# Kernel tuning notes

Measured on AMD Instinct MI355X. Metric: run time of the kernel, lower is better.

The kernel has to match this reference:

```python
import jax, jax.numpy as jnp
import numpy as np
import math

EMBED_DIM = 1024
NUM_HEADS = 16
HEAD_DIM = EMBED_DIM // NUM_HEADS
ROPE_BASE = 10000.0


def setup_inputs() -> dict:
    key = jax.random.key(0)
    ks = jax.random.split(key, 11)
    B, S, E = 2, 2048, EMBED_DIM
    s = 1.0 / math.sqrt(E)
    return {
        "query": jax.random.normal(ks[0], (B, S, E), jnp.float32),
        "key": jax.random.normal(ks[1], (B, S, E), jnp.float32),
        "value": jax.random.normal(ks[2], (B, S, E), jnp.float32),
        "Wq": jax.random.normal(ks[3], (E, E), jnp.float32) * s,
        "bq": jnp.zeros((E,), jnp.float32),
        "Wk": jax.random.normal(ks[4], (E, E), jnp.float32) * s,
        "bk": jnp.zeros((E,), jnp.float32),
        "Wv": jax.random.normal(ks[5], (E, E), jnp.float32) * s,
        "bv": jnp.zeros((E,), jnp.float32),
        "Wo": jax.random.normal(ks[6], (E, E), jnp.float32) * s,
        "bo": jnp.zeros((E,), jnp.float32),
    }


def _rope_cache(S, D, dtype):
    inv_freq = 1.0 / (ROPE_BASE ** (jnp.arange(0, D, 2, dtype=jnp.float32) / D))
    t = jnp.arange(S, dtype=jnp.float32)
    freqs = t[:, None] * inv_freq[None, :]  # [S, D/2]
    return jnp.cos(freqs).astype(dtype), jnp.sin(freqs).astype(dtype)


def _apply_rope(x, cos, sin):
    # x: [B, H, S, D]; cos/sin: [S, D/2]
    x_even = x[..., 0::2]
    x_odd = x[..., 1::2]
    rot_even = x_even * cos - x_odd * sin
    rot_odd = x_odd * cos + x_even * sin
    # interleave back: [..., D/2, 2] -> [..., D]
    return jnp.stack([rot_even, rot_odd], axis=-1).reshape(x.shape)


def reference(query, key, value, Wq, bq, Wk, bk, Wv, bv, Wo, bo):
    B, S, E = query.shape
    H, D = NUM_HEADS, HEAD_DIM
    q = (query @ Wq.T + bq).reshape(B, S, H, D).transpose(0, 2, 1, 3)
    k = (key @ Wk.T + bk).reshape(B, S, H, D).transpose(0, 2, 1, 3)
    v = (value @ Wv.T + bv).reshape(B, S, H, D).transpose(0, 2, 1, 3)
    cos, sin = _rope_cache(S, D, q.dtype)
    q = _apply_rope(q, cos, sin)
    k = _apply_rope(k, cos, sin)
    scores = jnp.einsum('bhsd,bhtd->bhst', q, k) / math.sqrt(D)
    attn = jax.nn.softmax(scores, axis=-1)
    out = jnp.einsum('bhst,bhtd->bhsd', attn, v)
    out = out.transpose(0, 2, 1, 3).reshape(B, S, E)
    return out @ Wo.T + bo
```

## Files before the change

### kernel.cpp

```cpp
#include <hip/hip_runtime.h>
#include <math.h>

typedef unsigned short u16;
typedef __bf16 bf16x8 __attribute__((ext_vector_type(8)));
typedef float floatx4 __attribute__((ext_vector_type(4)));
typedef float floatx16 __attribute__((ext_vector_type(16)));

#define MFMA16(a, b, c) __builtin_amdgcn_mfma_f32_16x16x32_bf16((a), (b), (c), 0, 0, 0)
#define MFMA32(a, b, c) __builtin_amdgcn_mfma_f32_32x32x16_bf16((a), (b), (c), 0, 0, 0)

__device__ __forceinline__ float bf2f(u16 u) {
  union { float f; unsigned int i; } v; v.i = ((unsigned int)u) << 16; return v.f;
}
__device__ __forceinline__ u16 f2bf(float f) {
  __bf16 h = (__bf16)f;
  union { __bf16 h; u16 u; } v; v.h = h; return v.u;
}
__device__ __forceinline__ bf16x8 cvt8(float4 a, float4 b) {
  bf16x8 r;
  r[0] = (__bf16)a.x; r[1] = (__bf16)a.y; r[2] = (__bf16)a.z; r[3] = (__bf16)a.w;
  r[4] = (__bf16)b.x; r[5] = (__bf16)b.y; r[6] = (__bf16)b.z; r[7] = (__bf16)b.w;
  return r;
}
__device__ __forceinline__ void gl2lds16(const void* g, void* l) {
  __builtin_amdgcn_global_load_lds(
      (const __attribute__((address_space(1))) unsigned int*)g,
      (__attribute__((address_space(3))) unsigned int*)l, 16, 0, 0);
}

struct CvtArgs { const float* src[3]; u16* dst[3]; };
__global__ __launch_bounds__(256) void cvt_kernel(CvtArgs a) {
  const float* s = a.src[blockIdx.z];
  u16* d = a.dst[blockIdx.z];
  const int i = (blockIdx.x * 256 + threadIdx.x) * 8;
  const float4 x = *reinterpret_cast<const float4*>(s + i);
  const float4 y = *reinterpret_cast<const float4*>(s + i + 4);
  *reinterpret_cast<bf16x8*>(&d[i]) = cvt8(x, y);
}

struct GemmArgs {
  const void* A[3];
  const void* W[3];
  const float* bias[3];
  void* C[3];
  int out_mode[3];
};

template <int BM, int ABF16, int WBF16>
__global__ __launch_bounds__(256) void gemm_nt(GemmArgs args) {
  const int N = 1024, K = 1024;

  const int NY = gridDim.y;
  const int lin = blockIdx.x + (blockIdx.y << 3) + blockIdx.z * (NY << 3);
  const int chunk = NY * gridDim.z;
  const int nid = (lin & 7) * chunk + (lin >> 3);
  const int z = nid / (NY << 3);
  const int rem = nid - z * (NY << 3);
  const int m0 = (rem >> 3) * BM, n0 = (rem & 7) * 128;

  const float* bias = args.bias[z];
  const int out_mode = args.out_mode[z];
  constexpr int MI = BM / 32;

  __shared__ __align__(16) char AsB[ABF16 ? BM * 64 : BM * 128];
  __shared__ __align__(16) char BsB[WBF16 ? 128 * 64 : 128 * 128];

  const int t = threadIdx.x;
  const int wave = t >> 6, lane = t & 63;
  const int lr = lane & 15, quad = lane >> 4;
  const int wm = (wave >> 1) * (BM / 2), wn = (wave & 1) * 64;

  auto stage = [&](int kt) {
    if constexpr (ABF16) {
      const u16* Ab = (const u16*)args.A[z];
      constexpr int NI = BM / 16;
#pragma unroll
      for (int j = 0; j < (NI + 3) / 4; j++) {
        const int ii = wave + j * 4;
        if (NI >= 4 || ii < NI) {
          const int r0 = ii * 16;
          const int row = r0 + (lane >> 2);
          const int cg = (lane & 3) ^ ((lane >> 2) & 3);
          gl2lds16(Ab + (size_t)(m0 + row) * K + kt + cg * 8, AsB + r0 * 64 + lane * 16);
        }
      }
    } else {
      const float* Af = (const float*)args.A[z];
#pragma unroll
      for (int j = 0; j < BM / 32; j++) {
        const int r0 = wave * (BM / 4) + j * 8;
        const int row = r0 + (lane >> 3);
        const int cg = (lane & 7) ^ ((lane >> 3) & 7);
        gl2lds16(Af + (size_t)(m0 + row) * K + kt + cg * 4, AsB + r0 * 128 + lane * 16);
      }
    }
    if constexpr (WBF16) {
      const u16* Wb = (const u16*)args.W[z];
#pragma unroll
      for (int j = 0; j < 2; j++) {
        const int r0 = (wave + j * 4) * 16;
        const int row = r0 + (lane >> 2);
        const int cg = (lane & 3) ^ ((lane >> 2) & 3);
        gl2lds16(Wb + (size_t)(n0 + row) * K + kt + cg * 8, BsB + r0 * 64 + lane * 16);
      }
    } else {
      const float* Wf = (const float*)args.W[z];
#pragma unroll
      for (int j = 0; j < 4; j++) {
        const int r0 = wave * 32 + j * 8;
        const int row = r0 + (lane >> 3);
        const int cg = (lane & 7) ^ ((lane >> 3) & 7);
        gl2lds16(Wf + (size_t)(n0 + row) * K + kt + cg * 4, BsB + r0 * 128 + lane * 16);
      }
    }
  };

  floatx4 acc[MI][4] = {};

  for (int kt = 0; kt < K; kt += 32) {
    __syncthreads();
    stage(kt);
    __syncthreads();

    bf16x8 af[MI], bf[4];
#pragma unroll
    for (int i = 0; i < MI; i++) {
      const int row = wm + i * 16 + lr;
      if constexpr (ABF16) {
        const int cp = quad ^ (row & 3);
        af[i] = *reinterpret_cast<const bf16x8*>(AsB + row * 64 + cp * 16);
      } else {
        const int e = row & 7;
        const float4 c0 = *reinterpret_cast<const float4*>(AsB + row * 128 + ((2 * quad) ^ e) * 16);
        const float4 c1 = *reinterpret_cast<const float4*>(AsB + row * 128 + ((2 * quad + 1) ^ e) * 16);
        af[i] = cvt8(c0, c1);
      }
    }
#pragma unroll
    for (int i = 0; i < 4; i++) {
      const int row = wn + i * 16 + lr;
      if constexpr (WBF16) {
        const int cp = quad ^ (row & 3);
        bf[i] = *reinterpret_cast<const bf16x8*>(BsB + row * 64 + cp * 16);
      } else {
        const int e = row & 7;
        const float4 c0 = *reinterpret_cast<const float4*>(BsB + row * 128 + ((2 * quad) ^ e) * 16);
        const float4 c1 = *reinterpret_cast<const float4*>(BsB + row * 128 + ((2 * quad + 1) ^ e) * 16);
        bf[i] = cvt8(c0, c1);
      }
    }
#pragma unroll
    for (int mi = 0; mi < MI; mi++)
#pragma unroll
      for (int nf = 0; nf < 4; nf++)
        acc[mi][nf] = MFMA16(af[mi], bf[nf], acc[mi][nf]);
  }

#pragma unroll
  for (int nf = 0; nf < 4; nf++) {
    const int col = n0 + wn + nf * 16 + lr;
    const float bv = bias[col];
#pragma unroll
    for (int mi = 0; mi < MI; mi++) {
      const int row0 = m0 + wm + mi * 16 + quad * 4;
      if (out_mode == 0) {
        u16* C = (u16*)args.C[z];
#pragma unroll
        for (int r = 0; r < 4; r++)
          C[(row0 + r) * N + col] = f2bf(acc[mi][nf][r] + bv);
      } else if (out_mode == 1) {
        u16* C = (u16*)args.C[z];
        const int h = col >> 6, d = col & 63;
        const int b = row0 >> 11, s = row0 & 2047;
        ushort4 pk;
        pk.x = f2bf(acc[mi][nf][0] + bv);
        pk.y = f2bf(acc[mi][nf][1] + bv);
        pk.z = f2bf(acc[mi][nf][2] + bv);
        pk.w = f2bf(acc[mi][nf][3] + bv);
        *reinterpret_cast<ushort4*>(&C[((b * 16 + h) * 64 + d) * 2048 + s]) = pk;
      } else {
        float* C = (float*)args.C[z];
#pragma unroll
        for (int r = 0; r < 4; r++)
          C[(row0 + r) * N + col] = acc[mi][nf][r] + bv;
      }
    }
  }
}

__global__ __launch_bounds__(256) void rope_kernel(u16* Q, u16* Kb) {
  const int idx = blockIdx.x * 256 + threadIdx.x;
  const int tensor = idx >> 19;
  const int i = idx & 524287;
  u16* P = tensor ? Kb : Q;
  const int row = i >> 7;
  const int cg = i & 127;
  const int s = row & 2047;
  const int col0 = cg * 8;
  const float scale = tensor ? 1.0f : 0.18033688011112042f;
  union { uint4 u; u16 h[8]; } v;
  v.u = *reinterpret_cast<const uint4*>(&P[row * 1024 + col0]);
  const int j0 = (col0 & 63) >> 1;
#pragma unroll
  for (int p = 0; p < 4; p++) {
    const int j = j0 + p;
    const float inv = exp2f(-(float)j * (13.287712379549449f / 32.0f));
    const float f = (float)s * inv;
    float sn, cs;
    sincosf(f, &sn, &cs);
    const float e = bf2f(v.h[2 * p]), o = bf2f(v.h[2 * p + 1]);
    v.h[2 * p]     = f2bf((e * cs - o * sn) * scale);
    v.h[2 * p + 1] = f2bf((o * cs + e * sn) * scale);
  }
  *reinterpret_cast<uint4*>(&P[row * 1024 + col0]) = v.u;
}

#define MAKE_PB(pp, g, out) do {                                              \
    unsigned int wA, wB, wC, wD;                                              \
    asm("v_cvt_pk_bf16_f32 %0, %1, %2" : "=v"(wA) : "v"((pp)[(g)+0]), "v"((pp)[(g)+1])); \
    asm("v_cvt_pk_bf16_f32 %0, %1, %2" : "=v"(wB) : "v"((pp)[(g)+4]), "v"((pp)[(g)+5])); \
    asm("v_cvt_pk_bf16_f32 %0, %1, %2" : "=v"(wC) : "v"((pp)[(g)+2]), "v"((pp)[(g)+3])); \
    asm("v_cvt_pk_bf16_f32 %0, %1, %2" : "=v"(wD) : "v"((pp)[(g)+6]), "v"((pp)[(g)+7])); \
    asm("v_permlane32_swap_b32 %0, %1" : "+v"(wA), "+v"(wB));                 \
    asm("v_permlane32_swap_b32 %0, %1" : "+v"(wC), "+v"(wD));                 \
    union { unsigned int w[4]; bf16x8 v; } u_;                                \
    u_.w[0] = wA; u_.w[1] = wC; u_.w[2] = wB; u_.w[3] = wD;                   \
    (out) = u_.v;                                                             \
  } while (0)

__global__ __launch_bounds__(256, 2) void attn_kernel(const u16* Q, const u16* K,
                                                      const u16* Vt, u16* O) {
  const int lin = blockIdx.x + (blockIdx.y << 4);
  const int nid = (lin & 7) * 64 + (lin >> 3);
  const int bx = nid & 15, bh = nid >> 4;

  const int b = bh >> 4, h = bh & 15;
  const int t = threadIdx.x;
  const int warp = t >> 6, lane = t & 63;
  const int lq = lane & 31, hi = lane >> 5;

  __shared__ __align__(16) u16 Ks[2][64][64];
  __shared__ __align__(16) u16 Vs[2][64][64];

  const int q0 = bx * 128 + warp * 32;

  const u16* qp = &Q[(size_t)(b * 2048 + q0 + lq) * 1024 + h * 64 + hi * 8];
  bf16x8 qf[4];
#pragma unroll
  for (int s = 0; s < 4; s++) qf[s] = *reinterpret_cast<const bf16x8*>(&qp[s * 16]);

  const u16* kbase = &K[(size_t)b * 2048 * 1024 + h * 64];
  const u16* vbase = &Vt[(size_t)bh * 131072];

  const int srr = lane >> 3;
  const int scg = (lane & 7) ^ srr;

  auto stage = [&](int kt2, int bufi) {
#pragma unroll
    for (int j = 0; j < 2; j++) {
      const int r0 = warp * 16 + j * 8;
      const int row = r0 + srr;
      gl2lds16(kbase + (size_t)(kt2 + row) * 1024 + scg * 8, &Ks[bufi][r0][0]);
      gl2lds16(vbase + (size_t)row * 2048 + kt2 + scg * 8, &Vs[bufi][r0][0]);
    }
  };

  floatx16 o0 = {}, o1 = {};
  float m = -1.0e30f, l = 0.0f;

  stage(0, 0);
  int buf = 0;
  for (int kt = 0; kt < 2048; kt += 64) {
    __syncthreads();
    if (kt + 64 < 2048) stage(kt + 64, buf ^ 1);

    bf16x8 kf[2][4], vf[4][2];
#pragma unroll
    for (int kb = 0; kb < 2; kb++) {
      const int r = kb * 32 + lq;
#pragma unroll
      for (int s = 0; s < 4; s++)
        kf[kb][s] = *reinterpret_cast<const bf16x8*>(&Ks[buf][r][((s * 2 + hi) ^ (r & 7)) * 8]);
    }
#pragma unroll
    for (int d = 0; d < 2; d++) {
      const int r = d * 32 + lq;
#pragma unroll
      for (int ks = 0; ks < 4; ks++)
        vf[ks][d] = *reinterpret_cast<const bf16x8*>(&Vs[buf][r][((ks * 2 + hi) ^ (r & 7)) * 8]);
    }

    floatx16 p0 = {}, p1 = {};
#pragma unroll
    for (int s = 0; s < 4; s++) {
      p0 = MFMA32(kf[0][s], qf[s], p0);
      p1 = MFMA32(kf[1][s], qf[s], p1);
    }

    float mx = p0[0];
#pragma unroll
    for (int r = 1; r < 16; r++) mx = fmaxf(mx, p0[r]);
#pragma unroll
    for (int r = 0; r < 16; r++) mx = fmaxf(mx, p1[r]);
    mx = fmaxf(mx, __shfl_xor(mx, 32, 64));
    if (!__all(mx <= m + 10.0f)) {
      const float mn = fmaxf(m, mx);
      const float al = __builtin_amdgcn_exp2f(m - mn);
      m = mn;
      l *= al;
#pragma unroll
      for (int r = 0; r < 16; r++) { o0[r] *= al; o1[r] *= al; }
    }
    float sum = 0.0f;
#pragma unroll
    for (int r = 0; r < 16; r++) { p0[r] = __builtin_amdgcn_exp2f(p0[r] - m); sum += p0[r]; }
#pragma unroll
    for (int r = 0; r < 16; r++) { p1[r] = __builtin_amdgcn_exp2f(p1[r] - m); sum += p1[r]; }
    l += sum + __shfl_xor(sum, 32, 64);

    bf16x8 pb0, pb1, pb2, pb3;
    MAKE_PB(p0, 0, pb0);
    MAKE_PB(p0, 8, pb1);
    MAKE_PB(p1, 0, pb2);
    MAKE_PB(p1, 8, pb3);

    o0 = MFMA32(vf[0][0], pb0, o0);
    o1 = MFMA32(vf[0][1], pb0, o1);
    o0 = MFMA32(vf[1][0], pb1, o0);
    o1 = MFMA32(vf[1][1], pb1, o1);
    o0 = MFMA32(vf[2][0], pb2, o0);
    o1 = MFMA32(vf[2][1], pb2, o1);
    o0 = MFMA32(vf[3][0], pb3, o0);
    o1 = MFMA32(vf[3][1], pb3, o1);

    buf ^= 1;
  }

  const float rl = 1.0f / l;
  u16* op = &O[(size_t)(b * 2048 + q0 + lq) * 1024 + h * 64 + hi * 4];
#pragma unroll
  for (int rq = 0; rq < 4; rq++) {
    ushort4 s0, s1;
    s0.x = f2bf(o0[4 * rq + 0] * rl); s0.y = f2bf(o0[4 * rq + 1] * rl);
    s0.z = f2bf(o0[4 * rq + 2] * rl); s0.w = f2bf(o0[4 * rq + 3] * rl);
    s1.x = f2bf(o1[4 * rq + 0] * rl); s1.y = f2bf(o1[4 * rq + 1] * rl);
    s1.z = f2bf(o1[4 * rq + 2] * rl); s1.w = f2bf(o1[4 * rq + 3] * rl);
    *reinterpret_cast<ushort4*>(&op[rq * 8]) = s0;
    *reinterpret_cast<ushort4*>(&op[rq * 8 + 32]) = s1;
  }
}

extern "C" void kernel_launch(void* const* d_in, const int* in_sizes, int n_in,
                              void* d_out, int out_size, void* d_ws, size_t ws_size,
                              hipStream_t stream) {
  (void)in_sizes; (void)n_in; (void)out_size;
  const float* query = (const float*)d_in[0];
  const float* key   = (const float*)d_in[1];
  const float* value = (const float*)d_in[2];
  const float* Wq = (const float*)d_in[3];
  const float* bq = (const float*)d_in[4];
  const float* Wk = (const float*)d_in[5];
  const float* bk = (const float*)d_in[6];
  const float* Wv = (const float*)d_in[7];
  const float* bv = (const float*)d_in[8];
  const float* Wo = (const float*)d_in[9];
  const float* bo = (const float*)d_in[10];

  u16* Qb = (u16*)d_ws;
  u16* Kb = (u16*)d_out;
  u16* Vt = (u16*)d_out + 4194304;

  const bool haveW = ws_size >= (size_t)(8388608 + 4 * 2097152);
  const bool haveA = ws_size >= (size_t)(8388608 + 4 * 2097152 + 25165824);
  u16* Wbf = (u16*)d_ws + 4194304;
  u16* Abf = (u16*)d_ws + 4194304 + 4194304;

  if (haveW) {
    CvtArgs cw;
    cw.src[0] = Wq; cw.dst[0] = Wbf;
    cw.src[1] = Wk; cw.dst[1] = Wbf + 1048576;
    cw.src[2] = Wv; cw.dst[2] = Wbf + 2097152;
    cvt_kernel<<<dim3(512, 1, 3), dim3(256), 0, stream>>>(cw);
    CvtArgs co;
    co.src[0] = Wo; co.dst[0] = Wbf + 3145728;
    co.src[1] = Wo; co.dst[1] = Wbf + 3145728;
    co.src[2] = Wo; co.dst[2] = Wbf + 3145728;
    cvt_kernel<<<dim3(512, 1, 1), dim3(256), 0, stream>>>(co);
  }
  if (haveA) {
    CvtArgs ca;
    ca.src[0] = query; ca.dst[0] = Abf;
    ca.src[1] = key;   ca.dst[1] = Abf + 4194304;
    ca.src[2] = value; ca.dst[2] = Abf + 8388608;
    cvt_kernel<<<dim3(2048, 1, 3), dim3(256), 0, stream>>>(ca);
  }

  GemmArgs g1;
  g1.bias[0] = bq; g1.C[0] = Qb; g1.out_mode[0] = 0;
  g1.bias[1] = bk; g1.C[1] = Kb; g1.out_mode[1] = 0;
  g1.bias[2] = bv; g1.C[2] = Vt; g1.out_mode[2] = 1;
  if (haveA) {
    g1.A[0] = Abf; g1.A[1] = Abf + 4194304; g1.A[2] = Abf + 8388608;
  } else {
    g1.A[0] = query; g1.A[1] = key; g1.A[2] = value;
  }
  if (haveW) {
    g1.W[0] = Wbf; g1.W[1] = Wbf + 1048576; g1.W[2] = Wbf + 2097152;
  } else {
    g1.W[0] = Wq; g1.W[1] = Wk; g1.W[2] = Wv;
  }
  if (haveA && haveW)
    gemm_nt<128, 1, 1><<<dim3(8, 32, 3), dim3(256), 0, stream>>>(g1);
  else if (haveW)
    gemm_nt<128, 0, 1><<<dim3(8, 32, 3), dim3(256), 0, stream>>>(g1);
  else
    gemm_nt<128, 0, 0><<<dim3(8, 32, 3), dim3(256), 0, stream>>>(g1);

  rope_kernel<<<dim3(4096), dim3(256), 0, stream>>>(Qb, Kb);

  attn_kernel<<<dim3(16, 32), dim3(256), 0, stream>>>(Qb, Kb, Vt, Qb);

  GemmArgs g2;
  for (int i = 0; i < 3; i++) {
    g2.A[i] = Qb; g2.bias[i] = bo;
    g2.C[i] = d_out; g2.out_mode[i] = 2;
    g2.W[i] = haveW ? (const void*)(Wbf + 3145728) : (const void*)Wo;
  }
  if (haveW)
    gemm_nt<64, 1, 1><<<dim3(8, 64, 1), dim3(256), 0, stream>>>(g2);
  else
    gemm_nt<64, 1, 0><<<dim3(8, 64, 1), dim3(256), 0, stream>>>(g2);
}
```

Before: 231.1 us.

## Fuse Q RoPE into attention, deepen K/V staging, merge weight conversions

RoPE and the softmax scale for Q are now applied to the Q fragments held in registers inside the attention kernel, so the standalone RoPE pass only touches K and does half the global traffic. The attention K/V LDS staging grows from two to four buffers, and each sync loads two 64-row tiles, halving barrier count. MFMA sections are wrapped in s_setprio hints. The four weight conversions are merged into one launch. The larger LDS footprint (64KB) may limit occupancy, and each attention block now recomputes sincos for its Q rows.

After: 227.9 us. About the same (-1.4%).

```diff
diff --git a/kernel.cpp b/kernel.cpp
--- a/kernel.cpp
+++ b/kernel.cpp
@@ -28,7 +28,7 @@
       (__attribute__((address_space(3))) unsigned int*)l, 16, 0, 0);
 }
 
-struct CvtArgs { const float* src[3]; u16* dst[3]; };
+struct CvtArgs { const float* src[4]; u16* dst[4]; };
 __global__ __launch_bounds__(256) void cvt_kernel(CvtArgs a) {
   const float* s = a.src[blockIdx.z];
   u16* d = a.dst[blockIdx.z];
@@ -188,18 +188,14 @@
   }
 }
 
-__global__ __launch_bounds__(256) void rope_kernel(u16* Q, u16* Kb) {
+__global__ __launch_bounds__(256) void rope_kernel(u16* Kb) {
   const int idx = blockIdx.x * 256 + threadIdx.x;
-  const int tensor = idx >> 19;
-  const int i = idx & 524287;
-  u16* P = tensor ? Kb : Q;
-  const int row = i >> 7;
-  const int cg = i & 127;
+  const int row = idx >> 7;
+  const int cg = idx & 127;
   const int s = row & 2047;
   const int col0 = cg * 8;
-  const float scale = tensor ? 1.0f : 0.18033688011112042f;
   union { uint4 u; u16 h[8]; } v;
-  v.u = *reinterpret_cast<const uint4*>(&P[row * 1024 + col0]);
+  v.u = *reinterpret_cast<const uint4*>(&Kb[row * 1024 + col0]);
   const int j0 = (col0 & 63) >> 1;
 #pragma unroll
   for (int p = 0; p < 4; p++) {
@@ -209,10 +205,10 @@
     float sn, cs;
     sincosf(f, &sn, &cs);
     const float e = bf2f(v.h[2 * p]), o = bf2f(v.h[2 * p + 1]);
-    v.h[2 * p]     = f2bf((e * cs - o * sn) * scale);
-    v.h[2 * p + 1] = f2bf((o * cs + e * sn) * scale);
-  }
-  *reinterpret_cast<uint4*>(&P[row * 1024 + col0]) = v.u;
+    v.h[2 * p]     = f2bf(e * cs - o * sn);
+    v.h[2 * p + 1] = f2bf(o * cs + e * sn);
+  }
+  *reinterpret_cast<uint4*>(&Kb[row * 1024 + col0]) = v.u;
 }
 
 #define MAKE_PB(pp, g, out) do {                                              \
@@ -239,8 +235,8 @@
   const int warp = t >> 6, lane = t & 63;
   const int lq = lane & 31, hi = lane >> 5;
 
-  __shared__ __align__(16) u16 Ks[2][64][64];
-  __shared__ __align__(16) u16 Vs[2][64][64];
+  __shared__ __align__(16) u16 Ks[4][64][64];
+  __shared__ __align__(16) u16 Vs[4][64][64];
 
   const int q0 = bx * 128 + warp * 32;
 
@@ -249,31 +245,43 @@
 #pragma unroll
   for (int s = 0; s < 4; s++) qf[s] = *reinterpret_cast<const bf16x8*>(&qp[s * 16]);
 
+  {
+    const float seqf = (float)(q0 + lq);
+#pragma unroll
+    for (int s = 0; s < 4; s++) {
+#pragma unroll
+      for (int p = 0; p < 4; p++) {
+        const int jp = s * 8 + hi * 4 + p;
+        const float inv = exp2f(-(float)jp * (13.287712379549449f / 32.0f));
+        float sn, cs;
+        sincosf(seqf * inv, &sn, &cs);
+        const float e = (float)qf[s][2 * p], o = (float)qf[s][2 * p + 1];
+        qf[s][2 * p]     = (__bf16)((e * cs - o * sn) * 0.18033688011112042f);
+        qf[s][2 * p + 1] = (__bf16)((o * cs + e * sn) * 0.18033688011112042f);
+      }
+    }
+  }
+
   const u16* kbase = &K[(size_t)b * 2048 * 1024 + h * 64];
   const u16* vbase = &Vt[(size_t)bh * 131072];
 
   const int srr = lane >> 3;
   const int scg = (lane & 7) ^ srr;
 
-  auto stage = [&](int kt2, int bufi) {
+  auto stage = [&](int kt2, int slot) {
 #pragma unroll
     for (int j = 0; j < 2; j++) {
       const int r0 = warp * 16 + j * 8;
       const int row = r0 + srr;
-      gl2lds16(kbase + (size_t)(kt2 + row) * 1024 + scg * 8, &Ks[bufi][r0][0]);
-      gl2lds16(vbase + (size_t)row * 2048 + kt2 + scg * 8, &Vs[bufi][r0][0]);
+      gl2lds16(kbase + (size_t)(kt2 + row) * 1024 + scg * 8, &Ks[slot][r0][0]);
+      gl2lds16(vbase + (size_t)row * 2048 + kt2 + scg * 8, &Vs[slot][r0][0]);
     }
   };
 
   floatx16 o0 = {}, o1 = {};
   float m = -1.0e30f, l = 0.0f;
 
-  stage(0, 0);
-  int buf = 0;
-  for (int kt = 0; kt < 2048; kt += 64) {
-    __syncthreads();
-    if (kt + 64 < 2048) stage(kt + 64, buf ^ 1);
-
+  auto compute = [&](int buf) {
     bf16x8 kf[2][4], vf[4][2];
 #pragma unroll
     for (int kb = 0; kb < 2; kb++) {
@@ -291,11 +299,13 @@
     }
 
     floatx16 p0 = {}, p1 = {};
+    __builtin_amdgcn_s_setprio(1);
 #pragma unroll
     for (int s = 0; s < 4; s++) {
       p0 = MFMA32(kf[0][s], qf[s], p0);
       p1 = MFMA32(kf[1][s], qf[s], p1);
     }
+    __builtin_amdgcn_s_setprio(0);
 
     float mx = p0[0];
 #pragma unroll
@@ -324,6 +334,7 @@
     MAKE_PB(p1, 0, pb2);
     MAKE_PB(p1, 8, pb3);
 
+    __builtin_amdgcn_s_setprio(1);
     o0 = MFMA32(vf[0][0], pb0, o0);
     o1 = MFMA32(vf[0][1], pb0, o1);
     o0 = MFMA32(vf[1][0], pb1, o0);
@@ -332,8 +343,20 @@
     o1 = MFMA32(vf[2][1], pb2, o1);
     o0 = MFMA32(vf[3][0], pb3, o0);
     o1 = MFMA32(vf[3][1], pb3, o1);
-
-    buf ^= 1;
+    __builtin_amdgcn_s_setprio(0);
+  };
+
+  stage(0, 0);
+  stage(64, 1);
+  for (int kt = 0; kt < 2048; kt += 128) {
+    const int s0 = (kt >> 6) & 3;
+    __syncthreads();
+    if (kt + 128 < 2048) {
+      stage(kt + 128, s0 ^ 2);
+      stage(kt + 192, (s0 ^ 2) | 1);
+    }
+    compute(s0);
+    compute(s0 | 1);
   }
 
   const float rl = 1.0f / l;
@@ -380,18 +403,15 @@
     cw.src[0] = Wq; cw.dst[0] = Wbf;
     cw.src[1] = Wk; cw.dst[1] = Wbf + 1048576;
     cw.src[2] = Wv; cw.dst[2] = Wbf + 2097152;
-    cvt_kernel<<<dim3(512, 1, 3), dim3(256), 0, stream>>>(cw);
-    CvtArgs co;
-    co.src[0] = Wo; co.dst[0] = Wbf + 3145728;
-    co.src[1] = Wo; co.dst[1] = Wbf + 3145728;
-    co.src[2] = Wo; co.dst[2] = Wbf + 3145728;
-    cvt_kernel<<<dim3(512, 1, 1), dim3(256), 0, stream>>>(co);
+    cw.src[3] = Wo; cw.dst[3] = Wbf + 3145728;
+    cvt_kernel<<<dim3(512, 1, 4), dim3(256), 0, stream>>>(cw);
   }
   if (haveA) {
     CvtArgs ca;
     ca.src[0] = query; ca.dst[0] = Abf;
     ca.src[1] = key;   ca.dst[1] = Abf + 4194304;
     ca.src[2] = value; ca.dst[2] = Abf + 8388608;
+    ca.src[3] = query; ca.dst[3] = Abf;
     cvt_kernel<<<dim3(2048, 1, 3), dim3(256), 0, stream>>>(ca);
   }
 
@@ -416,7 +436,7 @@
   else
     gemm_nt<128, 0, 0><<<dim3(8, 32, 3), dim3(256), 0, stream>>>(g1);
 
-  rope_kernel<<<dim3(4096), dim3(256), 0, stream>>>(Qb, Kb);
+  rope_kernel<<<dim3(2048), dim3(256), 0, stream>>>(Kb);
 
   attn_kernel<<<dim3(16, 32), dim3(256), 0, stream>>>(Qb, Kb, Vt, Qb);
 
```
